# Kernel optimization log

Measured on AMD Instinct MI355X. Metric: run time of the kernel, lower is better.

## Reference

```python
import jax, jax.numpy as jnp
import numpy as np

H = 10  # hidden_dim

def _lstm_layer(x_tbd, w_ih, w_hh, b_ih, b_hh):
    # x_tbd: [T, B, D]; w_ih: [4H, D]; w_hh: [4H, H]; biases [4H]
    B = x_tbd.shape[1]
    h0 = jnp.zeros((B, H), x_tbd.dtype)
    c0 = jnp.zeros((B, H), x_tbd.dtype)
    # precompute input projections for all timesteps: [T, B, 4H]
    xg = jnp.einsum('tbd,gd->tbg', x_tbd, w_ih) + b_ih + b_hh

    def step(carry, xg_t):
        h, c = carry
        gates = xg_t + h @ w_hh.T  # [B, 4H]
        i, f, g, o = jnp.split(gates, 4, axis=-1)  # torch gate order i,f,g,o
        i = jax.nn.sigmoid(i); f = jax.nn.sigmoid(f)
        g = jnp.tanh(g); o = jax.nn.sigmoid(o)
        c = f * c + i * g
        h = o * jnp.tanh(c)
        return (h, c), h

    (hT, cT), hs = jax.lax.scan(step, (h0, c0), xg)
    return hs, hT  # hs: [T, B, H]

def setup_inputs() -> dict:
    key = jax.random.key(0)
    ks = jax.random.split(key, 11)
    B, T, D = 32768, 28, 28
    s0 = 1.0 / np.sqrt(H)
    u = lambda k, shape: jax.random.uniform(k, shape, jnp.float32, -s0, s0)
    return {
        'x': jax.random.normal(ks[0], (B, T, D), jnp.float32),
        'w_ih0': u(ks[1], (4 * H, D)),
        'w_hh0': u(ks[2], (4 * H, H)),
        'b_ih0': u(ks[3], (4 * H,)),
        'b_hh0': u(ks[4], (4 * H,)),
        'w_ih1': u(ks[5], (4 * H, H)),
        'w_hh1': u(ks[6], (4 * H, H)),
        'b_ih1': u(ks[7], (4 * H,)),
        'b_hh1': u(ks[8], (4 * H,)),
        'w_cls': u(ks[9], (10, H)),
        'b_cls': u(ks[10], (10,)),
    }

def reference(x, w_ih0, w_hh0, b_ih0, b_hh0, w_ih1, w_hh1, b_ih1, b_hh1, w_cls, b_cls):
    x_tbd = jnp.swapaxes(x, 0, 1)  # [T, B, D]
    hs0, _ = _lstm_layer(x_tbd, w_ih0, w_hh0, b_ih0, b_hh0)
    _, hT1 = _lstm_layer(hs0, w_ih1, w_hh1, b_ih1, b_hh1)  # hT1 = h_n[-1]
    return hT1 @ w_cls.T + b_cls  # [B, 10]
```

## Files before the change

### kernel.cpp

```cpp
#include <hip/hip_runtime.h>


#define HDIM 10
#define DDIM 28
#define TSTEPS 28
#define NX 14

typedef __attribute__((ext_vector_type(8))) short short8;
typedef __attribute__((ext_vector_type(4))) float f32x4;

__device__ __forceinline__ unsigned short bf16_rne(float f) {
    unsigned u = __builtin_bit_cast(unsigned, f);
    u += 0x7FFFu + ((u >> 16) & 1u);
    return (unsigned short)(u >> 16);
}
__device__ __forceinline__ float bf16_f(unsigned short h) {
    unsigned u = ((unsigned)h) << 16;
    return __builtin_bit_cast(float, u);
}
__device__ __forceinline__ unsigned pk_hl(float v) {
    unsigned a, p;
    const float z = 0.0f;
    asm("v_cvt_pk_bf16_f32 %0, %1, %2" : "=v"(a) : "v"(v), "v"(z));
    const float hif = __builtin_bit_cast(float, a << 16);
    const float d = v - hif;
    asm("v_cvt_pk_bf16_f32 %0, %1, %2" : "=v"(p) : "v"(v), "v"(d));
    return p;
}
__device__ __forceinline__ float sig_f(float v) {
    return __builtin_amdgcn_rcpf(1.0f + __expf(-v));
}
__device__ __forceinline__ float tanh_f(float v) {
    return 2.0f * __builtin_amdgcn_rcpf(1.0f + __expf(-2.0f * v)) - 1.0f;
}

#define FENCE() __asm volatile("" ::: "memory")
#define WR32(arrp, sidx, val) (*(unsigned*)&(arrp)[(sidx)] = (val))


#define RDA(MH) do {                                                          \
    _Pragma("unroll")                                                         \
    for (int c = 0; c < 2; ++c)                                               \
        A1f[MH][c] = *(const short8*)&uA1w[(16 * (MH) + lm) * 72 + 32 * c + 8 * q]; \
    _Pragma("unroll")                                                         \
    for (int c = 0; c < 4; ++c)                                               \
        A0f[MH][c] = *(const short8*)&uA0w[(16 * (MH) + lm) * 136 + 32 * c + 8 * q]; \
} while (0)

#define CMP(MH) do {                                                          \
    f32x4 C_[4], D_[4];                                                       \
    _Pragma("unroll")                                                         \
    for (int T4 = 0; T4 < 4; ++T4) {                                          \
        f32x4 accD = {bias1[T4], bias1[T4], bias1[T4], bias1[T4]};            \
        _Pragma("unroll")                                                     \
        for (int c = 0; c < 2; ++c)                                           \
            accD = __builtin_amdgcn_mfma_f32_16x16x32_bf16(A1f[MH][c], B1[T4][c], accD, 0, 0, 0); \
        D_[T4] = accD;                                                        \
        f32x4 accC = {bias0[T4], bias0[T4], bias0[T4], bias0[T4]};            \
        _Pragma("unroll")                                                     \
        for (int c = 0; c < 4; ++c)                                           \
            accC = __builtin_amdgcn_mfma_f32_16x16x32_bf16(A0f[MH][c], B0[T4][c], accC, 0, 0, 0); \
        C_[T4] = accC;                                                        \
    }                                                                         \
    _Pragma("unroll")                                                         \
    for (int r = 0; r < 4; ++r) {                                             \
        const float i1 = sig_f(D_[0][r]);                                     \
        const float f1 = sig_f(D_[1][r]);                                     \
        const float g1 = tanh_f(D_[2][r]);                                    \
        const float o1 = sig_f(D_[3][r]);                                     \
        const float c1 = f1 * c1s[MH][r] + i1 * g1;                           \
        c1s[MH][r] = c1;                                                      \
        h1v[MH][r] = o1 * tanh_f(c1);                                         \
        const float i0 = sig_f(C_[0][r]);                                     \
        const float f0 = sig_f(C_[1][r]);                                     \
        const float g0 = tanh_f(C_[2][r]);                                    \
        const float o0 = sig_f(C_[3][r]);                                     \
        const float c0 = f0 * c0s[MH][r] + i0 * g0;                           \
        c0s[MH][r] = c0;                                                      \
        h0v[MH][r] = o0 * tanh_f(c0);                                         \
    }                                                                         \
} while (0)

#define WRH(MH) do {                                                          \
    if (lm < 10) {                                                            \
        _Pragma("unroll")                                                     \
        for (int r = 0; r < 4; ++r) {                                         \
            const int m = 16 * (MH) + 4 * q + r;                              \
            const unsigned p1 = pk_hl(h1v[MH][r]);                            \
            unsigned short* r1 = &uA1w[m * 72];                               \
            WR32(r1, 20 + 2 * lm, p1); r1[50 + lm] = (unsigned short)p1;      \
            const unsigned p0 = pk_hl(h0v[MH][r]);                            \
            WR32(r1, 2 * lm, p0);      r1[40 + lm] = (unsigned short)p0;      \
            unsigned short* r0 = &uA0w[m * 136];                              \
            WR32(r0, 56 + 2 * lm, p0); r0[104 + lm] = (unsigned short)p0;     \
        }                                                                     \
    }                                                                         \
} while (0)

#define BODY(P, Q, T, FIRST) do {                                             \
                                    \
    RDA(0);                                                                   \
    if (!(FIRST)) { WRH(1); }                                                 \
    FENCE();                                                                  \
                   \
    if ((T) < TSTEPS - 3) {                                                   \
        _Pragma("unroll")                                                     \
        for (int i = 0; i < NX; ++i) { xoff[i] += DDIM; Q[i] = x[xoff[i]]; }  \
    }                                                                         \
    CMP(0);                                                                   \
    RDA(1);                                                                   \
    FENCE();                                                                  \
                    \
    WRH(0);                                                                   \
    if ((T) < TSTEPS - 2) {                                                   \
        _Pragma("unroll")                                                     \
        for (int i = 0; i < NX; ++i) {                                        \
            const unsigned p = pk_hl(P[i]);                                   \
            WR32(uA0w, lofsA[i], p);                                          \
            uA0w[lofsB[i]] = (unsigned short)p;                               \
        }                                                                     \
    }                                                                         \
    CMP(1);                                                                   \
    FENCE();                                                                  \
} while (0)

__global__ __launch_bounds__(128, 1) void lstm2_mfma_kernel(
    const float* __restrict__ x,
    const float* __restrict__ w_ih0, const float* __restrict__ w_hh0,
    const float* __restrict__ b_ih0, const float* __restrict__ b_hh0,
    const float* __restrict__ w_ih1, const float* __restrict__ w_hh1,
    const float* __restrict__ b_ih1, const float* __restrict__ b_hh1,
    const float* __restrict__ w_cls, const float* __restrict__ b_cls,
    float* __restrict__ out)
{
    __shared__ __align__(16) unsigned short uA0s[2][32 * 136];
    __shared__ __align__(16) unsigned short uA1s[2][32 * 72];
    __shared__ __align__(16) float hfins[2][32 * 12];

    const int l   = threadIdx.x & 63;
    const int wid = threadIdx.x >> 6;
    const int lm  = l & 15;
    const int q   = l >> 4;
    const int sbase = (blockIdx.x * 2 + wid) * 32;

    unsigned short* const uA0w = uA0s[wid];
    unsigned short* const uA1w = uA1s[wid];
    float* const hfinw = hfins[wid];

    for (int i = l; i < 32 * 22; i += 64) uA0w[(i / 22) * 136 + 114 + (i % 22)] = 0;
    for (int i = l; i < 32 * 12; i += 64) uA1w[(i / 12) * 72 + 60 + (i % 12)] = 0;

    short8 B0[4][4], B1[4][2];
    const bool gvalid = (lm < 10);
    #pragma unroll
    for (int T = 0; T < 4; ++T) {
        const int g = 10 * T + lm;
        #pragma unroll
        for (int c = 0; c < 4; ++c) {
            #pragma unroll
            for (int j = 0; j < 8; ++j) {
                const int kk = 32 * c + 8 * q + j;
                unsigned short bits = 0;
                if (gvalid && kk < 114) {
                    if (kk < 76) {
                        const int j2 = kk >> 1;
                        const float w = (j2 < 28) ? w_ih0[g * 28 + j2]
                                                  : w_hh0[g * 10 + (j2 - 28)];
                        bits = bf16_rne(w);
                    } else {
                        const int d = kk - 76;
                        const float w = (d < 28) ? w_ih0[g * 28 + d]
                                                 : w_hh0[g * 10 + (d - 28)];
                        const unsigned short hi = bf16_rne(w);
                        bits = bf16_rne(w - bf16_f(hi));
                    }
                }
                B0[T][c][j] = (short)bits;
            }
        }
        #pragma unroll
        for (int c = 0; c < 2; ++c) {
            #pragma unroll
            for (int j = 0; j < 8; ++j) {
                const int kk = 32 * c + 8 * q + j;
                unsigned short bits = 0;
                if (gvalid && kk < 60) {
                    if (kk < 40) {
                        const int j2 = kk >> 1;
                        const float w = (j2 < 10) ? w_ih1[g * 10 + j2]
                                                  : w_hh1[g * 10 + (j2 - 10)];
                        bits = bf16_rne(w);
                    } else {
                        const int d = kk - 40;
                        const float w = (d < 10) ? w_ih1[g * 10 + d]
                                                 : w_hh1[g * 10 + (d - 10)];
                        const unsigned short hi = bf16_rne(w);
                        bits = bf16_rne(w - bf16_f(hi));
                    }
                }
                B1[T][c][j] = (short)bits;
            }
        }
    }

    float bias0[4], bias1[4];
    #pragma unroll
    for (int T = 0; T < 4; ++T) {
        const int g = 10 * T + lm;
        bias0[T] = gvalid ? (b_ih0[g] + b_hh0[g]) : 0.0f;
        bias1[T] = gvalid ? (b_ih1[g] + b_hh1[g]) : 0.0f;
    }

    int xoff[NX], lofsA[NX], lofsB[NX];
    float xA[NX], xB[NX];
    #pragma unroll
    for (int i = 0; i < NX; ++i) {
        const int f = l + 64 * i;
        const int sm = f / 28, d = f - 28 * sm;
        lofsA[i] = sm * 136 + 2 * d;
        lofsB[i] = sm * 136 + 76 + d;
        xoff[i] = (sbase + sm) * (TSTEPS * DDIM) + d;
        xA[i] = x[xoff[i]];
    }
    #pragma unroll
    for (int i = 0; i < NX; ++i) {
        const unsigned p = pk_hl(xA[i]);
        WR32(uA0w, lofsA[i], p);
        uA0w[lofsB[i]] = (unsigned short)p;
    }
    if (lm < 10) {
        #pragma unroll
        for (int mh = 0; mh < 2; ++mh) {
            #pragma unroll
            for (int r = 0; r < 4; ++r) {
                const int m = 16 * mh + 4 * q + r;
                unsigned short* r0 = &uA0w[m * 136];
                WR32(r0, 56 + 2 * lm, 0u); r0[104 + lm] = 0;
                unsigned short* r1 = &uA1w[m * 72];
                WR32(r1, 2 * lm, 0u);      r1[40 + lm] = 0;
                WR32(r1, 20 + 2 * lm, 0u); r1[50 + lm] = 0;
            }
        }
    }
    FENCE();

    float c0s[2][4] = {{0,0,0,0},{0,0,0,0}}, c1s[2][4] = {{0,0,0,0},{0,0,0,0}};
    float h1v[2][4] = {{0,0,0,0},{0,0,0,0}};
    float h0v[2][4];
    short8 A0f[2][4], A1f[2][2];

    #pragma unroll
    for (int i = 0; i < NX; ++i) { xoff[i] += DDIM; xA[i] = x[xoff[i]]; }

    #pragma unroll
    for (int mh = 0; mh < 2; ++mh)
        #pragma unroll
        for (int c = 0; c < 4; ++c)
            A0f[mh][c] = *(const short8*)&uA0w[(16 * mh + lm) * 136 + 32 * c + 8 * q];
    FENCE();
    #pragma unroll
    for (int i = 0; i < NX; ++i) { xoff[i] += DDIM; xB[i] = x[xoff[i]]; }
    {
        f32x4 C[2][4];
        #pragma unroll
        for (int mh = 0; mh < 2; ++mh) {
            #pragma unroll
            for (int T = 0; T < 4; ++T) {
                f32x4 acc = {bias0[T], bias0[T], bias0[T], bias0[T]};
                #pragma unroll
                for (int c = 0; c < 4; ++c)
                    acc = __builtin_amdgcn_mfma_f32_16x16x32_bf16(A0f[mh][c], B0[T][c], acc, 0, 0, 0);
                C[mh][T] = acc;
            }
        }
        #pragma unroll
        for (int mh = 0; mh < 2; ++mh) {
            #pragma unroll
            for (int r = 0; r < 4; ++r) {
                const float i0 = sig_f(C[mh][0][r]);
                const float f0 = sig_f(C[mh][1][r]);
                const float g0 = tanh_f(C[mh][2][r]);
                const float o0 = sig_f(C[mh][3][r]);
                const float c0 = f0 * c0s[mh][r] + i0 * g0;
                c0s[mh][r] = c0;
                h0v[mh][r] = o0 * tanh_f(c0);
            }
        }
        if (lm < 10) {
            #pragma unroll
            for (int mh = 0; mh < 2; ++mh) {
                #pragma unroll
                for (int r = 0; r < 4; ++r) {
                    const int m = 16 * mh + 4 * q + r;
                    const unsigned p0 = pk_hl(h0v[mh][r]);
                    unsigned short* r0 = &uA0w[m * 136];
                    WR32(r0, 56 + 2 * lm, p0); r0[104 + lm] = (unsigned short)p0;
                    unsigned short* r1 = &uA1w[m * 72];
                    WR32(r1, 2 * lm, p0);      r1[40 + lm] = (unsigned short)p0;
                }
            }
        }
        #pragma unroll
        for (int i = 0; i < NX; ++i) {
            const unsigned p = pk_hl(xA[i]);
            WR32(uA0w, lofsA[i], p);
            uA0w[lofsB[i]] = (unsigned short)p;
        }
    }
    FENCE();

    BODY(xB, xA, 0, 1);
    BODY(xA, xB, 1, 0);
    #pragma unroll 1
    for (int tp = 1; tp < 13; ++tp) {
        BODY(xB, xA, 2 * tp, 0);
        BODY(xA, xB, 2 * tp + 1, 0);
    }
    BODY(xB, xA, 26, 0);

    WRH(1);
    FENCE();

    {
        #pragma unroll
        for (int mh = 0; mh < 2; ++mh)
            #pragma unroll
            for (int c = 0; c < 2; ++c)
                A1f[mh][c] = *(const short8*)&uA1w[(16 * mh + lm) * 72 + 32 * c + 8 * q];
        FENCE();
        f32x4 D[2][4];
        #pragma unroll
        for (int mh = 0; mh < 2; ++mh) {
            #pragma unroll
            for (int T = 0; T < 4; ++T) {
                f32x4 acc = {bias1[T], bias1[T], bias1[T], bias1[T]};
                #pragma unroll
                for (int c = 0; c < 2; ++c)
                    acc = __builtin_amdgcn_mfma_f32_16x16x32_bf16(A1f[mh][c], B1[T][c], acc, 0, 0, 0);
                D[mh][T] = acc;
            }
        }
        #pragma unroll
        for (int mh = 0; mh < 2; ++mh) {
            #pragma unroll
            for (int r = 0; r < 4; ++r) {
                const float i1 = sig_f(D[mh][0][r]);
                const float f1 = sig_f(D[mh][1][r]);
                const float g1 = tanh_f(D[mh][2][r]);
                const float o1 = sig_f(D[mh][3][r]);
                const float c1 = f1 * c1s[mh][r] + i1 * g1;
                h1v[mh][r] = o1 * tanh_f(c1);
            }
        }
    }

    if (lm < 10) {
        #pragma unroll
        for (int mh = 0; mh < 2; ++mh)
            #pragma unroll
            for (int r = 0; r < 4; ++r)
                hfinw[(16 * mh + 4 * q + r) * 12 + lm] = h1v[mh][r];
    }
    FENCE();
    if (lm < 10) {
        float wc[10];
        #pragma unroll
        for (int j = 0; j < 10; ++j) wc[j] = w_cls[lm * 10 + j];
        const float bo = b_cls[lm];
        #pragma unroll
        for (int mh = 0; mh < 2; ++mh) {
            #pragma unroll
            for (int r = 0; r < 4; ++r) {
                const int m = 16 * mh + 4 * q + r;
                float acc = bo;
                #pragma unroll
                for (int j = 0; j < 10; ++j) acc += hfinw[m * 12 + j] * wc[j];
                out[(size_t)(sbase + m) * 10 + lm] = acc;
            }
        }
    }
}

extern "C" void kernel_launch(void* const* d_in, const int* in_sizes, int n_in,
                              void* d_out, int out_size, void* d_ws, size_t ws_size,
                              hipStream_t stream) {
    const float* x     = (const float*)d_in[0];
    const float* w_ih0 = (const float*)d_in[1];
    const float* w_hh0 = (const float*)d_in[2];
    const float* b_ih0 = (const float*)d_in[3];
    const float* b_hh0 = (const float*)d_in[4];
    const float* w_ih1 = (const float*)d_in[5];
    const float* w_hh1 = (const float*)d_in[6];
    const float* b_ih1 = (const float*)d_in[7];
    const float* b_hh1 = (const float*)d_in[8];
    const float* w_cls = (const float*)d_in[9];
    const float* b_cls = (const float*)d_in[10];
    float* out = (float*)d_out;

    const int B = in_sizes[0] / (TSTEPS * DDIM);
    const int grid = B / 64;

    hipLaunchKernelGGL(lstm2_mfma_kernel, dim3(grid), dim3(128), 0, stream,
                       x, w_ih0, w_hh0, b_ih0, b_hh0,
                       w_ih1, w_hh1, b_ih1, b_hh1,
                       w_cls, b_cls, out);
}
```

Measured before the change: 236.0 us.

## Process 64 sequences per wave with a four-stage ring pipeline

Each block becomes a single wave handling 64 sequences as four 16-row M-tiles instead of two waves of 32. The timestep body becomes a four-phase ring that rotates LDS reads, MFMA compute and h writes across the tiles, so each tile's dependent-chain latency is hidden behind work on the other three. The x prefetch changes from double-buffered 14 loads to a single 28-load buffer. Register pressure roughly doubles (A fragments, states, x buffer), which risks spills, and there are now half as many waves on the GPU, giving less latency hiding between waves.

Measured after the change: 315.4 us. 33.7% more time.

```diff
diff --git a/kernel.cpp b/kernel.cpp
--- a/kernel.cpp
+++ b/kernel.cpp
@@ -4,7 +4,7 @@
 #define HDIM 10
 #define DDIM 28
 #define TSTEPS 28
-#define NX 14
+#define NX 28
 
 typedef __attribute__((ext_vector_type(8))) short short8;
 typedef __attribute__((ext_vector_type(4))) float f32x4;
@@ -97,34 +97,46 @@
     }                                                                         \
 } while (0)
 
-#define BODY(P, Q, T, FIRST) do {                                             \
-                                    \
-    RDA(0);                                                                   \
-    if (!(FIRST)) { WRH(1); }                                                 \
+#define XLOAD() do {                                                          \
+    _Pragma("unroll")                                                         \
+    for (int i = 0; i < NX; ++i) { xoff[i] += DDIM; xN[i] = x[xoff[i]]; }     \
+} while (0)
+
+#define XWRITE() do {                                                         \
+    _Pragma("unroll")                                                         \
+    for (int i = 0; i < NX; ++i) {                                            \
+        const unsigned p = pk_hl(xN[i]);                                      \
+        WR32(uA0w, lofsA[i], p);                                              \
+        uA0w[lofsB[i]] = (unsigned short)p;                                   \
+    }                                                                         \
+} while (0)
+
+#define RING(T, FIRST) do {                                                   \
+                     \
+    if (!(FIRST)) { WRH(3); }                                                 \
+    RDA(1);                                                                   \
+    if ((T) < TSTEPS - 2) { XLOAD(); }                                        \
+    CMP(0);                                                                   \
     FENCE();                                                                  \
-                   \
-    if ((T) < TSTEPS - 3) {                                                   \
-        _Pragma("unroll")                                                     \
-        for (int i = 0; i < NX; ++i) { xoff[i] += DDIM; Q[i] = x[xoff[i]]; }  \
-    }                                                                         \
-    CMP(0);                                                                   \
-    RDA(1);                                                                   \
-    FENCE();                                                                  \
-                    \
+                                      \
     WRH(0);                                                                   \
-    if ((T) < TSTEPS - 2) {                                                   \
-        _Pragma("unroll")                                                     \
-        for (int i = 0; i < NX; ++i) {                                        \
-            const unsigned p = pk_hl(P[i]);                                   \
-            WR32(uA0w, lofsA[i], p);                                          \
-            uA0w[lofsB[i]] = (unsigned short)p;                               \
-        }                                                                     \
-    }                                                                         \
+    RDA(2);                                                                   \
     CMP(1);                                                                   \
     FENCE();                                                                  \
-} while (0)
-
-__global__ __launch_bounds__(128, 1) void lstm2_mfma_kernel(
+     \
+    RDA(3);                                                                   \
+    WRH(1);                                                                   \
+    if ((T) < TSTEPS - 2) { XWRITE(); }                                       \
+    CMP(2);                                                                   \
+    FENCE();                                                                  \
+                                    \
+    WRH(2);                                                                   \
+    RDA(0);                                                                   \
+    CMP(3);                                                                   \
+    FENCE();                                                                  \
+} while (0)
+
+__global__ __launch_bounds__(64, 1) void lstm2_mfma_kernel(
     const float* __restrict__ x,
     const float* __restrict__ w_ih0, const float* __restrict__ w_hh0,
     const float* __restrict__ b_ih0, const float* __restrict__ b_hh0,
@@ -133,22 +145,17 @@
     const float* __restrict__ w_cls, const float* __restrict__ b_cls,
     float* __restrict__ out)
 {
-    __shared__ __align__(16) unsigned short uA0s[2][32 * 136];
-    __shared__ __align__(16) unsigned short uA1s[2][32 * 72];
-    __shared__ __align__(16) float hfins[2][32 * 12];
-
-    const int l   = threadIdx.x & 63;
-    const int wid = threadIdx.x >> 6;
-    const int lm  = l & 15;
-    const int q   = l >> 4;
-    const int sbase = (blockIdx.x * 2 + wid) * 32;
-
-    unsigned short* const uA0w = uA0s[wid];
-    unsigned short* const uA1w = uA1s[wid];
-    float* const hfinw = hfins[wid];
-
-    for (int i = l; i < 32 * 22; i += 64) uA0w[(i / 22) * 136 + 114 + (i % 22)] = 0;
-    for (int i = l; i < 32 * 12; i += 64) uA1w[(i / 12) * 72 + 60 + (i % 12)] = 0;
+    __shared__ __align__(16) unsigned short uA0w[64 * 136];
+    __shared__ __align__(16) unsigned short uA1w[64 * 72];
+    __shared__ __align__(16) float hfinw[64 * 12];
+
+    const int l  = threadIdx.x;
+    const int lm = l & 15;
+    const int q  = l >> 4;
+    const int sbase = blockIdx.x * 64;
+
+    for (int i = l; i < 64 * 22; i += 64) uA0w[(i / 22) * 136 + 114 + (i % 22)] = 0;
+    for (int i = l; i < 64 * 12; i += 64) uA1w[(i / 12) * 72 + 60 + (i % 12)] = 0;
 
     short8 B0[4][4], B1[4][2];
     const bool gvalid = (lm < 10);
@@ -212,7 +219,7 @@
     }
 
     int xoff[NX], lofsA[NX], lofsB[NX];
-    float xA[NX], xB[NX];
+    float xN[NX];
     #pragma unroll
     for (int i = 0; i < NX; ++i) {
         const int f = l + 64 * i;
@@ -220,17 +227,12 @@
         lofsA[i] = sm * 136 + 2 * d;
         lofsB[i] = sm * 136 + 76 + d;
         xoff[i] = (sbase + sm) * (TSTEPS * DDIM) + d;
-        xA[i] = x[xoff[i]];
-    }
-    #pragma unroll
-    for (int i = 0; i < NX; ++i) {
-        const unsigned p = pk_hl(xA[i]);
-        WR32(uA0w, lofsA[i], p);
-        uA0w[lofsB[i]] = (unsigned short)p;
-    }
+        xN[i] = x[xoff[i]];
+    }
+    XWRITE();
     if (lm < 10) {
         #pragma unroll
-        for (int mh = 0; mh < 2; ++mh) {
+        for (int mh = 0; mh < 4; ++mh) {
             #pragma unroll
             for (int r = 0; r < 4; ++r) {
                 const int m = 16 * mh + 4 * q + r;
@@ -244,119 +246,100 @@
     }
     FENCE();
 
-    float c0s[2][4] = {{0,0,0,0},{0,0,0,0}}, c1s[2][4] = {{0,0,0,0},{0,0,0,0}};
-    float h1v[2][4] = {{0,0,0,0},{0,0,0,0}};
-    float h0v[2][4];
-    short8 A0f[2][4], A1f[2][2];
-
-    #pragma unroll
-    for (int i = 0; i < NX; ++i) { xoff[i] += DDIM; xA[i] = x[xoff[i]]; }
-
-    #pragma unroll
-    for (int mh = 0; mh < 2; ++mh)
+    float c0s[4][4] = {{0,0,0,0},{0,0,0,0},{0,0,0,0},{0,0,0,0}};
+    float c1s[4][4] = {{0,0,0,0},{0,0,0,0},{0,0,0,0},{0,0,0,0}};
+    float h1v[4][4] = {{0,0,0,0},{0,0,0,0},{0,0,0,0},{0,0,0,0}};
+    float h0v[4][4];
+    short8 A0f[4][4], A1f[4][2];
+
+    XLOAD();
+
+    #pragma unroll
+    for (int mh = 0; mh < 4; ++mh)
         #pragma unroll
         for (int c = 0; c < 4; ++c)
             A0f[mh][c] = *(const short8*)&uA0w[(16 * mh + lm) * 136 + 32 * c + 8 * q];
     FENCE();
     #pragma unroll
-    for (int i = 0; i < NX; ++i) { xoff[i] += DDIM; xB[i] = x[xoff[i]]; }
-    {
-        f32x4 C[2][4];
-        #pragma unroll
-        for (int mh = 0; mh < 2; ++mh) {
-            #pragma unroll
-            for (int T = 0; T < 4; ++T) {
-                f32x4 acc = {bias0[T], bias0[T], bias0[T], bias0[T]};
-                #pragma unroll
-                for (int c = 0; c < 4; ++c)
-                    acc = __builtin_amdgcn_mfma_f32_16x16x32_bf16(A0f[mh][c], B0[T][c], acc, 0, 0, 0);
-                C[mh][T] = acc;
-            }
-        }
-        #pragma unroll
-        for (int mh = 0; mh < 2; ++mh) {
+    for (int mh = 0; mh < 4; ++mh) {
+        f32x4 C_[4];
+        #pragma unroll
+        for (int T = 0; T < 4; ++T) {
+            f32x4 acc = {bias0[T], bias0[T], bias0[T], bias0[T]};
+            #pragma unroll
+            for (int c = 0; c < 4; ++c)
+                acc = __builtin_amdgcn_mfma_f32_16x16x32_bf16(A0f[mh][c], B0[T][c], acc, 0, 0, 0);
+            C_[T] = acc;
+        }
+        #pragma unroll
+        for (int r = 0; r < 4; ++r) {
+            const float i0 = sig_f(C_[0][r]);
+            const float f0 = sig_f(C_[1][r]);
+            const float g0 = tanh_f(C_[2][r]);
+            const float o0 = sig_f(C_[3][r]);
+            const float c0 = f0 * c0s[mh][r] + i0 * g0;
+            c0s[mh][r] = c0;
+            h0v[mh][r] = o0 * tanh_f(c0);
+        }
+    }
+    if (lm < 10) {
+        #pragma unroll
+        for (int mh = 0; mh < 4; ++mh) {
             #pragma unroll
             for (int r = 0; r < 4; ++r) {
-                const float i0 = sig_f(C[mh][0][r]);
-                const float f0 = sig_f(C[mh][1][r]);
-                const float g0 = tanh_f(C[mh][2][r]);
-                const float o0 = sig_f(C[mh][3][r]);
-                const float c0 = f0 * c0s[mh][r] + i0 * g0;
-                c0s[mh][r] = c0;
-                h0v[mh][r] = o0 * tanh_f(c0);
-            }
-        }
-        if (lm < 10) {
-            #pragma unroll
-            for (int mh = 0; mh < 2; ++mh) {
-                #pragma unroll
-                for (int r = 0; r < 4; ++r) {
-                    const int m = 16 * mh + 4 * q + r;
-                    const unsigned p0 = pk_hl(h0v[mh][r]);
-                    unsigned short* r0 = &uA0w[m * 136];
-                    WR32(r0, 56 + 2 * lm, p0); r0[104 + lm] = (unsigned short)p0;
-                    unsigned short* r1 = &uA1w[m * 72];
-                    WR32(r1, 2 * lm, p0);      r1[40 + lm] = (unsigned short)p0;
-                }
-            }
-        }
-        #pragma unroll
-        for (int i = 0; i < NX; ++i) {
-            const unsigned p = pk_hl(xA[i]);
-            WR32(uA0w, lofsA[i], p);
-            uA0w[lofsB[i]] = (unsigned short)p;
-        }
-    }
-    FENCE();
-
-    BODY(xB, xA, 0, 1);
-    BODY(xA, xB, 1, 0);
+                const int m = 16 * mh + 4 * q + r;
+                const unsigned p0 = pk_hl(h0v[mh][r]);
+                unsigned short* r0 = &uA0w[m * 136];
+                WR32(r0, 56 + 2 * lm, p0); r0[104 + lm] = (unsigned short)p0;
+                unsigned short* r1 = &uA1w[m * 72];
+                WR32(r1, 2 * lm, p0);      r1[40 + lm] = (unsigned short)p0;
+            }
+        }
+    }
+    XWRITE();
+    FENCE();
+    RDA(0);
+    FENCE();
+
+    RING(0, 1);
     #pragma unroll 1
-    for (int tp = 1; tp < 13; ++tp) {
-        BODY(xB, xA, 2 * tp, 0);
-        BODY(xA, xB, 2 * tp + 1, 0);
-    }
-    BODY(xB, xA, 26, 0);
-
-    WRH(1);
-    FENCE();
-
-    {
-        #pragma unroll
-        for (int mh = 0; mh < 2; ++mh)
+    for (int t = 1; t < TSTEPS - 1; ++t) {
+        RING(t, 0);
+    }
+    WRH(3);
+    FENCE();
+
+    #pragma unroll
+    for (int mh = 0; mh < 4; ++mh)
+        #pragma unroll
+        for (int c = 0; c < 2; ++c)
+            A1f[mh][c] = *(const short8*)&uA1w[(16 * mh + lm) * 72 + 32 * c + 8 * q];
+    FENCE();
+    #pragma unroll
+    for (int mh = 0; mh < 4; ++mh) {
+        f32x4 D_[4];
+        #pragma unroll
+        for (int T = 0; T < 4; ++T) {
+            f32x4 acc = {bias1[T], bias1[T], bias1[T], bias1[T]};
             #pragma unroll
             for (int c = 0; c < 2; ++c)
-                A1f[mh][c] = *(const short8*)&uA1w[(16 * mh + lm) * 72 + 32 * c + 8 * q];
-        FENCE();
-        f32x4 D[2][4];
-        #pragma unroll
-        for (int mh = 0; mh < 2; ++mh) {
-            #pragma unroll
-            for (int T = 0; T < 4; ++T) {
-                f32x4 acc = {bias1[T], bias1[T], bias1[T], bias1[T]};
-                #pragma unroll
-                for (int c = 0; c < 2; ++c)
-                    acc = __builtin_amdgcn_mfma_f32_16x16x32_bf16(A1f[mh][c], B1[T][c], acc, 0, 0, 0);
-                D[mh][T] = acc;
-            }
-        }
-        #pragma unroll
-        for (int mh = 0; mh < 2; ++mh) {
-            #pragma unroll
-            for (int r = 0; r < 4; ++r) {
-                const float i1 = sig_f(D[mh][0][r]);
-                const float f1 = sig_f(D[mh][1][r]);
-                const float g1 = tanh_f(D[mh][2][r]);
-                const float o1 = sig_f(D[mh][3][r]);
-                const float c1 = f1 * c1s[mh][r] + i1 * g1;
-                h1v[mh][r] = o1 * tanh_f(c1);
-            }
+                acc = __builtin_amdgcn_mfma_f32_16x16x32_bf16(A1f[mh][c], B1[T][c], acc, 0, 0, 0);
+            D_[T] = acc;
+        }
+        #pragma unroll
+        for (int r = 0; r < 4; ++r) {
+            const float i1 = sig_f(D_[0][r]);
+            const float f1 = sig_f(D_[1][r]);
+            const float g1 = tanh_f(D_[2][r]);
+            const float o1 = sig_f(D_[3][r]);
+            const float c1 = f1 * c1s[mh][r] + i1 * g1;
+            h1v[mh][r] = o1 * tanh_f(c1);
         }
     }
 
     if (lm < 10) {
         #pragma unroll
-        for (int mh = 0; mh < 2; ++mh)
+        for (int mh = 0; mh < 4; ++mh)
             #pragma unroll
             for (int r = 0; r < 4; ++r)
                 hfinw[(16 * mh + 4 * q + r) * 12 + lm] = h1v[mh][r];
@@ -368,7 +351,7 @@
         for (int j = 0; j < 10; ++j) wc[j] = w_cls[lm * 10 + j];
         const float bo = b_cls[lm];
         #pragma unroll
-        for (int mh = 0; mh < 2; ++mh) {
+        for (int mh = 0; mh < 4; ++mh) {
             #pragma unroll
             for (int r = 0; r < 4; ++r) {
                 const int m = 16 * mh + 4 * q + r;
@@ -400,7 +383,7 @@
     const int B = in_sizes[0] / (TSTEPS * DDIM);
     const int grid = B / 64;
 
-    hipLaunchKernelGGL(lstm2_mfma_kernel, dim3(grid), dim3(128), 0, stream,
+    hipLaunchKernelGGL(lstm2_mfma_kernel, dim3(grid), dim3(64), 0, stream,
                        x, w_ih0, w_hh0, b_ih0, b_hh0,
                        w_ih1, w_hh1, b_ih1, b_hh1,
                        w_cls, b_cls, out);
```

## Merge layer-0 and layer-1 LDS operand buffers into one shared row layout

Applied to the files above, without the earlier changes.

Combines the two per-wave LDS A-operand arrays (layer 0 with stride 136 and layer 1 with stride 72) into a single stride-168 row. The layer-1 operands become an overlapping window of the same row, so h0 is written once per step instead of twice to separate buffers, which cuts LDS store count in WRH. In exchange, the layer-0 MFMA K dimension grows from 4 to 5 chunks, since zero gaps and the h1 slot now sit inside its window. That adds MFMAs per step, more B0 registers and more LDS read traffic.

After: 234.9 us. Within noise of the previous version (-0.5%).

```diff
diff --git a/kernel.cpp b/kernel.cpp
--- a/kernel.cpp
+++ b/kernel.cpp
@@ -5,6 +5,13 @@
 #define DDIM 28
 #define TSTEPS 28
 #define NX 14
+#define STR 168
+#define ZH0P 56
+#define ZH1P 76
+#define ZH0H 96
+#define ZH1H 106
+#define ZXH  116
+#define ZPAD 144
 
 typedef __attribute__((ext_vector_type(8))) short short8;
 typedef __attribute__((ext_vector_type(4))) float f32x4;
@@ -41,10 +48,10 @@
 #define RDA(MH) do {                                                          \
     _Pragma("unroll")                                                         \
     for (int c = 0; c < 2; ++c)                                               \
-        A1f[MH][c] = *(const short8*)&uA1w[(16 * (MH) + lm) * 72 + 32 * c + 8 * q]; \
+        A1f[MH][c] = *(const short8*)&uAw[(16 * (MH) + lm) * STR + ZH0P + 32 * c + 8 * q]; \
     _Pragma("unroll")                                                         \
-    for (int c = 0; c < 4; ++c)                                               \
-        A0f[MH][c] = *(const short8*)&uA0w[(16 * (MH) + lm) * 136 + 32 * c + 8 * q]; \
+    for (int c = 0; c < 5; ++c)                                               \
+        A0f[MH][c] = *(const short8*)&uAw[(16 * (MH) + lm) * STR + 32 * c + 8 * q]; \
 } while (0)
 
 #define CMP(MH) do {                                                          \
@@ -58,7 +65,7 @@
         D_[T4] = accD;                                                        \
         f32x4 accC = {bias0[T4], bias0[T4], bias0[T4], bias0[T4]};            \
         _Pragma("unroll")                                                     \
-        for (int c = 0; c < 4; ++c)                                           \
+        for (int c = 0; c < 5; ++c)                                           \
             accC = __builtin_amdgcn_mfma_f32_16x16x32_bf16(A0f[MH][c], B0[T4][c], accC, 0, 0, 0); \
         C_[T4] = accC;                                                        \
     }                                                                         \
@@ -86,13 +93,11 @@
         _Pragma("unroll")                                                     \
         for (int r = 0; r < 4; ++r) {                                         \
             const int m = 16 * (MH) + 4 * q + r;                              \
+            unsigned short* rw = &uAw[m * STR];                               \
             const unsigned p1 = pk_hl(h1v[MH][r]);                            \
-            unsigned short* r1 = &uA1w[m * 72];                               \
-            WR32(r1, 20 + 2 * lm, p1); r1[50 + lm] = (unsigned short)p1;      \
+            WR32(rw, ZH1P + 2 * lm, p1); rw[ZH1H + lm] = (unsigned short)p1;  \
             const unsigned p0 = pk_hl(h0v[MH][r]);                            \
-            WR32(r1, 2 * lm, p0);      r1[40 + lm] = (unsigned short)p0;      \
-            unsigned short* r0 = &uA0w[m * 136];                              \
-            WR32(r0, 56 + 2 * lm, p0); r0[104 + lm] = (unsigned short)p0;     \
+            WR32(rw, ZH0P + 2 * lm, p0); rw[ZH0H + lm] = (unsigned short)p0;  \
         }                                                                     \
     }                                                                         \
 } while (0)
@@ -116,8 +121,8 @@
         _Pragma("unroll")                                                     \
         for (int i = 0; i < NX; ++i) {                                        \
             const unsigned p = pk_hl(P[i]);                                   \
-            WR32(uA0w, lofsA[i], p);                                          \
-            uA0w[lofsB[i]] = (unsigned short)p;                               \
+            WR32(uAw, lofsA[i], p);                                           \
+            uAw[lofsB[i]] = (unsigned short)p;                                \
         }                                                                     \
     }                                                                         \
     CMP(1);                                                                   \
@@ -133,8 +138,7 @@
     const float* __restrict__ w_cls, const float* __restrict__ b_cls,
     float* __restrict__ out)
 {
-    __shared__ __align__(16) unsigned short uA0s[2][32 * 136];
-    __shared__ __align__(16) unsigned short uA1s[2][32 * 72];
+    __shared__ __align__(16) unsigned short uAs[2][32 * STR];
     __shared__ __align__(16) float hfins[2][32 * 12];
 
     const int l   = threadIdx.x & 63;
@@ -143,34 +147,37 @@
     const int q   = l >> 4;
     const int sbase = (blockIdx.x * 2 + wid) * 32;
 
-    unsigned short* const uA0w = uA0s[wid];
-    unsigned short* const uA1w = uA1s[wid];
+    unsigned short* const uAw = uAs[wid];
     float* const hfinw = hfins[wid];
 
-    for (int i = l; i < 32 * 22; i += 64) uA0w[(i / 22) * 136 + 114 + (i % 22)] = 0;
-    for (int i = l; i < 32 * 12; i += 64) uA1w[(i / 12) * 72 + 60 + (i % 12)] = 0;
-
-    short8 B0[4][4], B1[4][2];
+    for (int i = l; i < 32 * 24; i += 64) uAw[(i / 24) * STR + ZPAD + (i % 24)] = 0;
+
+    short8 B0[4][5], B1[4][2];
     const bool gvalid = (lm < 10);
     #pragma unroll
     for (int T = 0; T < 4; ++T) {
         const int g = 10 * T + lm;
         #pragma unroll
-        for (int c = 0; c < 4; ++c) {
+        for (int c = 0; c < 5; ++c) {
             #pragma unroll
             for (int j = 0; j < 8; ++j) {
                 const int kk = 32 * c + 8 * q + j;
                 unsigned short bits = 0;
-                if (gvalid && kk < 114) {
-                    if (kk < 76) {
-                        const int j2 = kk >> 1;
-                        const float w = (j2 < 28) ? w_ih0[g * 28 + j2]
-                                                  : w_hh0[g * 10 + (j2 - 28)];
-                        bits = bf16_rne(w);
-                    } else {
-                        const int d = kk - 76;
-                        const float w = (d < 28) ? w_ih0[g * 28 + d]
-                                                 : w_hh0[g * 10 + (d - 28)];
+                if (gvalid) {
+                    if (kk < ZH0P) {
+                        bits = bf16_rne(w_ih0[g * 28 + (kk >> 1)]);
+                    } else if (kk < ZH1P) {
+                        bits = bf16_rne(w_hh0[g * 10 + ((kk - ZH0P) >> 1)]);
+                    } else if (kk < ZH0H) {
+                        bits = 0;
+                    } else if (kk < ZH1H) {
+                        const float w = w_hh0[g * 10 + (kk - ZH0H)];
+                        const unsigned short hi = bf16_rne(w);
+                        bits = bf16_rne(w - bf16_f(hi));
+                    } else if (kk < ZXH) {
+                        bits = 0;
+                    } else if (kk < ZPAD) {
+                        const float w = w_ih0[g * 28 + (kk - ZXH)];
                         const unsigned short hi = bf16_rne(w);
                         bits = bf16_rne(w - bf16_f(hi));
                     }
@@ -185,15 +192,16 @@
                 const int kk = 32 * c + 8 * q + j;
                 unsigned short bits = 0;
                 if (gvalid && kk < 60) {
-                    if (kk < 40) {
-                        const int j2 = kk >> 1;
-                        const float w = (j2 < 10) ? w_ih1[g * 10 + j2]
-                                                  : w_hh1[g * 10 + (j2 - 10)];
-                        bits = bf16_rne(w);
+                    if (kk < 20) {
+                        bits = bf16_rne(w_ih1[g * 10 + (kk >> 1)]);
+                    } else if (kk < 40) {
+                        bits = bf16_rne(w_hh1[g * 10 + ((kk - 20) >> 1)]);
+                    } else if (kk < 50) {
+                        const float w = w_ih1[g * 10 + (kk - 40)];
+                        const unsigned short hi = bf16_rne(w);
+                        bits = bf16_rne(w - bf16_f(hi));
                     } else {
-                        const int d = kk - 40;
-                        const float w = (d < 10) ? w_ih1[g * 10 + d]
-                                                 : w_hh1[g * 10 + (d - 10)];
+                        const float w = w_hh1[g * 10 + (kk - 50)];
                         const unsigned short hi = bf16_rne(w);
                         bits = bf16_rne(w - bf16_f(hi));
                     }
@@ -217,28 +225,25 @@
     for (int i = 0; i < NX; ++i) {
         const int f = l + 64 * i;
         const int sm = f / 28, d = f - 28 * sm;
-        lofsA[i] = sm * 136 + 2 * d;
-        lofsB[i] = sm * 136 + 76 + d;
+        lofsA[i] = sm * STR + 2 * d;
+        lofsB[i] = sm * STR + ZXH + d;
         xoff[i] = (sbase + sm) * (TSTEPS * DDIM) + d;
         xA[i] = x[xoff[i]];
     }
     #pragma unroll
     for (int i = 0; i < NX; ++i) {
         const unsigned p = pk_hl(xA[i]);
-        WR32(uA0w, lofsA[i], p);
-        uA0w[lofsB[i]] = (unsigned short)p;
+        WR32(uAw, lofsA[i], p);
+        uAw[lofsB[i]] = (unsigned short)p;
     }
     if (lm < 10) {
         #pragma unroll
         for (int mh = 0; mh < 2; ++mh) {
             #pragma unroll
             for (int r = 0; r < 4; ++r) {
-                const int m = 16 * mh + 4 * q + r;
-                unsigned short* r0 = &uA0w[m * 136];
-                WR32(r0, 56 + 2 * lm, 0u); r0[104 + lm] = 0;
-                unsigned short* r1 = &uA1w[m * 72];
-                WR32(r1, 2 * lm, 0u);      r1[40 + lm] = 0;
-                WR32(r1, 20 + 2 * lm, 0u); r1[50 + lm] = 0;
+                unsigned short* rw = &uAw[(16 * mh + 4 * q + r) * STR];
+                WR32(rw, ZH0P + 2 * lm, 0u); rw[ZH0H + lm] = 0;
+                WR32(rw, ZH1P + 2 * lm, 0u); rw[ZH1H + lm] = 0;
             }
         }
     }
@@ -247,7 +252,7 @@
     float c0s[2][4] = {{0,0,0,0},{0,0,0,0}}, c1s[2][4] = {{0,0,0,0},{0,0,0,0}};
     float h1v[2][4] = {{0,0,0,0},{0,0,0,0}};
     float h0v[2][4];
-    short8 A0f[2][4], A1f[2][2];
+    short8 A0f[2][5], A1f[2][2];
 
     #pragma unroll
     for (int i = 0; i < NX; ++i) { xoff[i] += DDIM; xA[i] = x[xoff[i]]; }
@@ -255,8 +260,8 @@
     #pragma unroll
     for (int mh = 0; mh < 2; ++mh)
         #pragma unroll
-        for (int c = 0; c < 4; ++c)
-            A0f[mh][c] = *(const short8*)&uA0w[(16 * mh + lm) * 136 + 32 * c + 8 * q];
+        for (int c = 0; c < 5; ++c)
+            A0f[mh][c] = *(const short8*)&uAw[(16 * mh + lm) * STR + 32 * c + 8 * q];
     FENCE();
     #pragma unroll
     for (int i = 0; i < NX; ++i) { xoff[i] += DDIM; xB[i] = x[xoff[i]]; }
@@ -268,7 +273,7 @@
             for (int T = 0; T < 4; ++T) {
                 f32x4 acc = {bias0[T], bias0[T], bias0[T], bias0[T]};
                 #pragma unroll
-                for (int c = 0; c < 4; ++c)
+                for (int c = 0; c < 5; ++c)
                     acc = __builtin_amdgcn_mfma_f32_16x16x32_bf16(A0f[mh][c], B0[T][c], acc, 0, 0, 0);
                 C[mh][T] = acc;
             }
@@ -291,20 +296,17 @@
             for (int mh = 0; mh < 2; ++mh) {
                 #pragma unroll
                 for (int r = 0; r < 4; ++r) {
-                    const int m = 16 * mh + 4 * q + r;
+                    unsigned short* rw = &uAw[(16 * mh + 4 * q + r) * STR];
                     const unsigned p0 = pk_hl(h0v[mh][r]);
-                    unsigned short* r0 = &uA0w[m * 136];
-                    WR32(r0, 56 + 2 * lm, p0); r0[104 + lm] = (unsigned short)p0;
-                    unsigned short* r1 = &uA1w[m * 72];
-                    WR32(r1, 2 * lm, p0);      r1[40 + lm] = (unsigned short)p0;
+                    WR32(rw, ZH0P + 2 * lm, p0); rw[ZH0H + lm] = (unsigned short)p0;
                 }
             }
         }
         #pragma unroll
         for (int i = 0; i < NX; ++i) {
             const unsigned p = pk_hl(xA[i]);
-            WR32(uA0w, lofsA[i], p);
-            uA0w[lofsB[i]] = (unsigned short)p;
+            WR32(uAw, lofsA[i], p);
+            uAw[lofsB[i]] = (unsigned short)p;
         }
     }
     FENCE();
@@ -326,7 +328,7 @@
         for (int mh = 0; mh < 2; ++mh)
             #pragma unroll
             for (int c = 0; c < 2; ++c)
-                A1f[mh][c] = *(const short8*)&uA1w[(16 * mh + lm) * 72 + 32 * c + 8 * q];
+                A1f[mh][c] = *(const short8*)&uAw[(16 * mh + lm) * STR + ZH0P + 32 * c + 8 * q];
         FENCE();
         f32x4 D[2][4];
         #pragma unroll
```
